# Kernel tuning notes

Hardware: AMD Instinct MI355X
Metric: run time of the kernel (lower is better)

## Reference

```python
import jax, jax.numpy as jnp
import numpy as np

E = 1_000_000      # edges in batch
N_BATCH = 50_000   # local nodes in batch
N_TOTAL = 100_000  # total entities
R = 1000           # num relations
D = 200            # rnn_in_dim == rnn_hid_dim


def setup_inputs() -> dict:
    key = jax.random.key(0)
    ks = jax.random.split(key, 9)
    s = 1.0 / np.sqrt(D)  # torch GRU init scale
    return {
        "edge_index": jax.random.randint(ks[0], (2, E), 0, N_BATCH),
        "edge_type": jax.random.randint(ks[1], (E,), 0, R),
        "node_id": jax.random.randint(ks[2], (N_BATCH,), 0, N_TOTAL),
        "static_entity_emb": jax.random.normal(ks[3], (N_TOTAL, D), jnp.float32),
        "dynamic_relation_emb": jax.random.normal(ks[4], (R, 1, D, 2), jnp.float32),
        "W_ih": jax.random.uniform(ks[5], (3 * D, D), jnp.float32, -s, s),
        "W_hh": jax.random.uniform(ks[6], (3 * D, D), jnp.float32, -s, s),
        "b_ih": jax.random.uniform(ks[7], (3 * D,), jnp.float32, -s, s),
        "b_hh": jax.random.uniform(ks[8], (3 * D,), jnp.float32, -s, s),
    }


def _scatter_mean_by_rel(emb, edge_type):
    # emb: [E, D] gathered entity embeddings; segment-mean over relation type -> [R, D]
    seg_sum = jax.ops.segment_sum(emb, edge_type, num_segments=R)
    cnt = jax.ops.segment_sum(jnp.ones((emb.shape[0], 1), emb.dtype), edge_type, num_segments=R)
    return jnp.where(cnt > 0, seg_sum / jnp.maximum(cnt, 1.0), 0.0)


def _gru_cell(x, h, W_ih, W_hh, b_ih, b_hh):
    # torch GRU gate order: r, z, n. x,h: [R, D]
    gi = x @ W_ih.T + b_ih
    gh = h @ W_hh.T + b_hh
    i_r, i_z, i_n = jnp.split(gi, 3, axis=-1)
    h_r, h_z, h_n = jnp.split(gh, 3, axis=-1)
    r = jax.nn.sigmoid(i_r + h_r)
    z = jax.nn.sigmoid(i_z + h_z)
    n = jnp.tanh(i_n + r * h_n)
    return (1.0 - z) * n + z * h


def reference(edge_index, edge_type, node_id, static_entity_emb,
              dynamic_relation_emb, W_ih, W_hh, b_ih, b_hh):
    src_nid = node_id[edge_index[0]]  # [E]
    dst_nid = node_id[edge_index[1]]  # [E]
    # gather + scatter-mean by relation (irregular access; the hot path)
    x_src = _scatter_mean_by_rel(static_entity_emb[src_nid], edge_type)  # [R, D]
    x_dst = _scatter_mean_by_rel(static_entity_emb[dst_nid], edge_type)  # [R, D]
    # single-layer hidden states per relation (side 0 = src, 1 = dst)
    h_src = dynamic_relation_emb[:, 0, :, 0]  # [R, D]
    h_dst = dynamic_relation_emb[:, 0, :, 1]  # [R, D]
    new_src = _gru_cell(x_src, h_src, W_ih, W_hh, b_ih, b_hh)
    new_dst = _gru_cell(x_dst, h_dst, W_ih, W_hh, b_ih, b_hh)
    # [R, num_layers=1, D, 2]
    return jnp.stack([new_src, new_dst], axis=-1)[:, None, :, :]
```

## Files before the change

kernel.cpp:

```cpp
#include <hip/hip_runtime.h>
#include <hip/hip_fp16.h>
#include <math.h>

#define DD     200
#define DD3    600
#define NBK    256
#define GB     256
#define SCH    8192
#define SCAP   11264
#define CHUNK  1024
#define KP     232
#define MP     2048
#define NP     640

typedef unsigned int   uint32;
typedef unsigned short uint16;
typedef __attribute__((ext_vector_type(8))) short bf16x8;
typedef __attribute__((ext_vector_type(4))) float f32x4;

static __device__ inline float bf2f(uint16 u) {
    union { uint32 i; float f; } x; x.i = ((uint32)u) << 16; return x.f;
}
static __device__ inline uint16 f2bf(float f) {
    union { float f; uint32 i; } x; x.f = f;
    return (uint16)((x.i + 0x7FFFu + ((x.i >> 16) & 1u)) >> 16);
}
static __device__ inline float asf(uint32 u) {
    union { uint32 i; float f; } x; x.i = u; return x.f;
}
static __device__ inline uint32 packbf(float a, float b) {
    return (uint32)f2bf(a) | ((uint32)f2bf(b) << 16);
}
static __device__ inline uint32 packh2(float a, float b) {
    __half2 h = __floats2half2_rn(a, b);
    union { __half2 h; uint32 u; } x; x.h = h; return x.u;
}
static __device__ inline __half2 ash2(uint32 u) {
    union { uint32 u; __half2 h; } x; x.u = u; return x.h;
}

__global__ void zero_kernel(int* __restrict__ cnt, int n) {
    int stride = gridDim.x * blockDim.x;
    for (int i = blockIdx.x * blockDim.x + threadIdx.x; i < n; i += stride) cnt[i] = 0;
}

__global__ void zerof_kernel(float* __restrict__ p, int n) {
    int stride = gridDim.x * blockDim.x;
    for (int i = blockIdx.x * blockDim.x + threadIdx.x; i < n; i += stride) p[i] = 0.f;
}

__launch_bounds__(512)
__global__ void blockhist_kernel(const int* __restrict__ etype, const int* __restrict__ eidx,
                                 int* __restrict__ boff, int E) {
    __shared__ int lc[NBK];
    const int tid = threadIdx.x;
    if (tid < NBK) lc[tid] = 0;
    __syncthreads();
    int per = (E + GB - 1) / GB;
    int beg = blockIdx.x * per;
    int end = min(E, beg + per);
    for (int e = beg + tid; e < end; e += 512) {
        int r  = etype[e];
        int ch = r >> 5;
        atomicAdd(&lc[(ch << 3) | (eidx[e] >> 13)], 1);
        atomicAdd(&lc[(ch << 3) | (eidx[E + e] >> 13)], 1);
    }
    __syncthreads();
    if (tid < NBK) boff[blockIdx.x * NBK + tid] = lc[tid];
}

__launch_bounds__(NBK)
__global__ void offscan_kernel(int* __restrict__ boff, int* __restrict__ offs256) {
    __shared__ int tot[NBK];
    __shared__ int s[NBK];
    const int t = threadIdx.x;
    int acc = 0;
    for (int b = 0; b < GB; ++b) {
        int v = boff[b * NBK + t];
        boff[b * NBK + t] = acc;
        acc += v;
    }
    tot[t] = acc;
    s[t] = acc;
    for (int off = 1; off < NBK; off <<= 1) {
        __syncthreads();
        int tmp = (t >= off) ? s[t - off] : 0;
        __syncthreads();
        s[t] += tmp;
    }
    __syncthreads();
    int base = s[t] - tot[t];
    offs256[t] = base;
    if (t == NBK - 1) offs256[NBK] = s[t];
    for (int b = 0; b < GB; ++b) boff[b * NBK + t] += base;
}

__launch_bounds__(512)
__global__ void blocksort_kernel(const int* __restrict__ etype, const int* __restrict__ eidx,
                                 const int* __restrict__ boff, uint32* __restrict__ binned,
                                 int E) {
    __shared__ uint32 raw[SCH];
    __shared__ uint32 srt[SCH];
    __shared__ int lhist[NBK];
    __shared__ int loff[NBK + 1];
    __shared__ int lcur[NBK];
    __shared__ int bbase[NBK];
    const int tid  = threadIdx.x;
    const int wv   = tid >> 6;
    const int lane = tid & 63;

    if (tid < NBK) bbase[tid] = boff[blockIdx.x * NBK + tid];
    int per = (E + GB - 1) / GB;
    int ebeg = blockIdx.x * per;
    int eend = min(E, ebeg + per);

    for (int cb = ebeg; cb < eend; cb += SCH / 2) {
        const int ne = min(SCH / 2, eend - cb);
        const int m  = 2 * ne;
        if (tid < NBK) lhist[tid] = 0;
        __syncthreads();
        for (int i = tid; i < ne; i += 512) {
            int e  = cb + i;
            int r  = etype[e];
            int sS = eidx[e];
            int sD = eidx[E + e];
            int ch = r >> 5;
            int rb = (r & 31) << 1;
            raw[2 * i]     = ((uint32)ch << 24) | ((uint32)rb << 16) | (uint32)sS;
            raw[2 * i + 1] = ((uint32)ch << 24) | ((uint32)(rb + 1) << 16) | (uint32)sD;
            atomicAdd(&lhist[(ch << 3) | (sS >> 13)], 1);
            atomicAdd(&lhist[(ch << 3) | (sD >> 13)], 1);
        }
        __syncthreads();
        if (tid == 0) {
            int acc = 0;
            for (int q = 0; q < NBK; ++q) { loff[q] = acc; acc += lhist[q]; }
            loff[NBK] = acc;
        }
        __syncthreads();
        if (tid < NBK) lcur[tid] = loff[tid];
        __syncthreads();
        for (int i = tid; i < m; i += 512) {
            uint32 pk = raw[i];
            int k = (int)((pk >> 24) << 3) | (int)((pk & 0xFFFFu) >> 13);
            int pos = atomicAdd(&lcur[k], 1);
            srt[pos] = pk;
        }
        __syncthreads();
        for (int b = wv; b < NBK; b += 8) {
            int lo = loff[b];
            int c  = loff[b + 1] - lo;
            if (c > 0) {
                int dst = bbase[b];
                for (int i = lane; i < c; i += 64) binned[dst + i] = srt[lo + i];
                if (lane == 0) bbase[b] = dst + c;
            }
        }
        __syncthreads();
    }
}

__launch_bounds__(512)
__global__ void sortbucket_kernel(const uint32* __restrict__ binned,
                                  const int* __restrict__ offs256,
                                  uint16* __restrict__ list, int* __restrict__ offs16k,
                                  int total) {
    __shared__ uint16 sorted[SCAP];
    __shared__ int hist[64];
    __shared__ int cur[64];
    __shared__ int scn[65];
    const int bk  = blockIdx.x;
    const int tid = threadIdx.x;
    const int beg = offs256[bk];
    const int end = offs256[bk + 1];
    const int len = end - beg;

    if (tid < 64) hist[tid] = 0;
    __syncthreads();
    for (int i = tid; i < len; i += 512)
        atomicAdd(&hist[(binned[beg + i] >> 16) & 63], 1);
    __syncthreads();
    if (tid == 0) {
        int acc = 0;
        #pragma unroll
        for (int q = 0; q < 64; ++q) { scn[q] = acc; cur[q] = acc; acc += hist[q]; }
        scn[64] = acc;
    }
    __syncthreads();
    if (tid < 64) offs16k[bk * 64 + tid] = beg + scn[tid];
    if (bk == 0 && tid == 64) offs16k[NBK * 64] = total;

    if (len <= SCAP) {
        for (int i = tid; i < len; i += 512) {
            uint32 e = binned[beg + i];
            int p = atomicAdd(&cur[(e >> 16) & 63], 1);
            sorted[p] = (uint16)(e & 0xFFFF);
        }
        __syncthreads();
        for (int i = tid; i < len; i += 512) list[beg + i] = sorted[i];
    } else {
        for (int i = tid; i < len; i += 512) {
            uint32 e = binned[beg + i];
            int p = atomicAdd(&cur[(e >> 16) & 63], 1);
            list[beg + p] = (uint16)(e & 0xFFFF);
        }
    }
}

__global__ void compact_kernel(const int* __restrict__ node_id, const float* __restrict__ emb,
                               uint32* __restrict__ cmp, int NB) {
    int idx = blockIdx.x * blockDim.x + threadIdx.x;
    if (idx >= NB * 50) return;
    int s = idx / 50, q = idx - s * 50;
    int nid = node_id[s];
    float4 v = *(const float4*)(emb + (size_t)nid * DD + 4 * q);
    *(uint2*)(cmp + (size_t)s * 100 + 2 * q) = make_uint2(packh2(v.x, v.y), packh2(v.z, v.w));
}

__launch_bounds__(256)
__global__ void partial7_kernel(const uint16* __restrict__ list,
                                const uint32* __restrict__ cmp,
                                const int* __restrict__ offs16k,
                                uint16* __restrict__ partial) {
    const int g    = blockIdx.x & 7;
    const int rest = blockIdx.x >> 3;
    const int rsl  = rest & 63;
    const int ch   = rest >> 6;
    const int b16  = ((ch * 8 + g) << 6) | rsl;
    const int tid  = threadIdx.x;
    const int w    = tid >> 6;
    const int lane = tid & 63;
    const int sub  = lane / 25;
    const int w25  = lane % 25;
    const int laneOff = w25 * 4;

    __shared__ uint16 sl[CHUNK];
    __shared__ float  red[8][DD];

    const int beg = offs16k[b16];
    const int end = offs16k[b16 + 1];

    __half2 h0 = __floats2half2_rn(0.f, 0.f);
    __half2 h1 = h0, h2 = h0, h3 = h0;

    for (int base = beg; base < end; base += CHUNK) {
        const int m = min(CHUNK, end - base);
        for (int i = tid; i < m; i += 256) sl[i] = list[base + i];
        __syncthreads();
        if (sub < 2) {
            int i = w * 2 + sub;
            for (; i + 24 < m; i += 32) {
                int s0 = sl[i];
                int s1 = sl[i + 8];
                int s2 = sl[i + 16];
                int s3 = sl[i + 24];
                uint4 v0 = *(const uint4*)(cmp + (size_t)s0 * 100 + laneOff);
                uint4 v1 = *(const uint4*)(cmp + (size_t)s1 * 100 + laneOff);
                uint4 v2 = *(const uint4*)(cmp + (size_t)s2 * 100 + laneOff);
                uint4 v3 = *(const uint4*)(cmp + (size_t)s3 * 100 + laneOff);
                h0 = __hadd2(h0, __hadd2(__hadd2(ash2(v0.x), ash2(v1.x)),
                                         __hadd2(ash2(v2.x), ash2(v3.x))));
                h1 = __hadd2(h1, __hadd2(__hadd2(ash2(v0.y), ash2(v1.y)),
                                         __hadd2(ash2(v2.y), ash2(v3.y))));
                h2 = __hadd2(h2, __hadd2(__hadd2(ash2(v0.z), ash2(v1.z)),
                                         __hadd2(ash2(v2.z), ash2(v3.z))));
                h3 = __hadd2(h3, __hadd2(__hadd2(ash2(v0.w), ash2(v1.w)),
                                         __hadd2(ash2(v2.w), ash2(v3.w))));
            }
            for (; i < m; i += 8) {
                int s0 = sl[i];
                uint4 v0 = *(const uint4*)(cmp + (size_t)s0 * 100 + laneOff);
                h0 = __hadd2(h0, ash2(v0.x));
                h1 = __hadd2(h1, ash2(v0.y));
                h2 = __hadd2(h2, ash2(v0.z));
                h3 = __hadd2(h3, ash2(v0.w));
            }
        }
        __syncthreads();
    }

    if (sub < 2) {
        int row = w * 2 + sub;
        int c = w25 * 8;
        red[row][c]     = __low2float(h0);  red[row][c + 1] = __high2float(h0);
        red[row][c + 2] = __low2float(h1);  red[row][c + 3] = __high2float(h1);
        red[row][c + 4] = __low2float(h2);  red[row][c + 5] = __high2float(h2);
        red[row][c + 6] = __low2float(h3);  red[row][c + 7] = __high2float(h3);
    }
    __syncthreads();

    if (tid < DD) {
        float s = 0.f;
        #pragma unroll
        for (int q = 0; q < 8; ++q) s += red[q][tid];
        partial[(size_t)b16 * DD + tid] = f2bf(s);
    }
}

__global__ void prep2_kernel(const uint16* __restrict__ partial,
                             const int* __restrict__ offs16k,
                             const float* __restrict__ dyn,
                             const float* __restrict__ W_ih, const float* __restrict__ W_hh,
                             uint32* __restrict__ Xb, uint32* __restrict__ Hb,
                             uint32* __restrict__ Wib, uint32* __restrict__ Whb, int RS2) {
    const int KU = KP / 2;
    int idx = blockIdx.x * blockDim.x + threadIdx.x;
    int XU = MP * KU, WU = NP * KU;
    const uint32* pp = (const uint32*)partial;
    if (idx < XU) {
        int row = idx / KU, kk = (idx - row * KU) * 2;
        uint32 o = 0;
        if (row < RS2 && kk < DD) {
            int ch = row >> 6, rsl = row & 63;
            float s0 = 0.f, s1 = 0.f;
            int n = 0;
            #pragma unroll
            for (int g = 0; g < 8; ++g) {
                int b16 = ((ch * 8 + g) << 6) | rsl;
                n += offs16k[b16 + 1] - offs16k[b16];
                uint32 v = pp[b16 * 100 + (kk >> 1)];
                s0 += asf(v << 16);
                s1 += asf(v & 0xFFFF0000u);
            }
            float rc = (n > 0) ? 1.f / (float)n : 0.f;
            o = packbf(s0 * rc, s1 * rc);
        }
        Xb[idx] = o;
    } else if (idx < 2 * XU) {
        int k2 = idx - XU;
        int row = k2 / KU, kk = (k2 - row * KU) * 2;
        uint32 o = 0;
        if (row < RS2 && kk < DD) {
            int r = row >> 1, side = row & 1;
            float h0 = dyn[((size_t)r * DD + kk) * 2 + side];
            float h1 = dyn[((size_t)r * DD + kk + 1) * 2 + side];
            o = packbf(h0, h1);
        }
        Hb[k2] = o;
    } else if (idx < 2 * XU + 2 * WU) {
        int k2 = idx - 2 * XU;
        const float* W = (k2 < WU) ? W_ih : W_hh;
        uint32* dst = (k2 < WU) ? Wib : Whb;
        if (k2 >= WU) k2 -= WU;
        int row = k2 / KU, kk = (k2 - row * KU) * 2;
        uint32 o = 0;
        if (row < DD3 && kk < DD) {
            o = packbf(W[(size_t)row * DD + kk], W[(size_t)row * DD + kk + 1]);
        }
        dst[k2] = o;
    }
}

__launch_bounds__(256)
__global__ void mfma_gates_kernel(const uint32* __restrict__ Xb, const uint32* __restrict__ Hb,
                                  const uint32* __restrict__ Wib, const uint32* __restrict__ Whb,
                                  float* __restrict__ G) {
    __shared__ short As[64 * KP];
    __shared__ short Bs[64 * KP];
    const int nt  = blockIdx.x;
    const int mt  = blockIdx.y;
    const int z   = blockIdx.z;
    const int tid = threadIdx.x;

    const uint32* Asrc = (z ? Hb : Xb) + (size_t)mt * 64 * (KP / 2);
    const uint32* Bsrc = (z ? Whb : Wib) + (size_t)nt * 64 * (KP / 2);
    {
        const uint4* a4 = (const uint4*)Asrc;
        const uint4* b4 = (const uint4*)Bsrc;
        uint4* la = (uint4*)As;
        uint4* lb = (uint4*)Bs;
        const int n16 = 64 * KP * 2 / 16;
        for (int i = tid; i < n16; i += 256) { la[i] = a4[i]; lb[i] = b4[i]; }
    }
    __syncthreads();

    const int w    = tid >> 6;
    const int lane = tid & 63;
    const int qm   = (w & 1) * 32;
    const int qn   = (w >> 1) * 32;
    const int lr   = lane & 15;
    const int lk   = (lane >> 4) * 8;

    f32x4 acc00 = {0.f, 0.f, 0.f, 0.f}, acc01 = acc00, acc10 = acc00, acc11 = acc00;
    #pragma unroll
    for (int ks = 0; ks < 7; ++ks) {
        int kof = ks * 32 + lk;
        bf16x8 a0 = *(const bf16x8*)&As[(qm + lr) * KP + kof];
        bf16x8 a1 = *(const bf16x8*)&As[(qm + 16 + lr) * KP + kof];
        bf16x8 b0 = *(const bf16x8*)&Bs[(qn + lr) * KP + kof];
        bf16x8 b1 = *(const bf16x8*)&Bs[(qn + 16 + lr) * KP + kof];
        acc00 = __builtin_amdgcn_mfma_f32_16x16x32_bf16(a0, b0, acc00, 0, 0, 0);
        acc01 = __builtin_amdgcn_mfma_f32_16x16x32_bf16(a0, b1, acc01, 0, 0, 0);
        acc10 = __builtin_amdgcn_mfma_f32_16x16x32_bf16(a1, b0, acc10, 0, 0, 0);
        acc11 = __builtin_amdgcn_mfma_f32_16x16x32_bf16(a1, b1, acc11, 0, 0, 0);
    }

    float* Gz = G + (size_t)z * MP * NP;
    const int mb = mt * 64 + qm + (lane >> 4) * 4;
    const int nb = nt * 64 + qn + lr;
    #pragma unroll
    for (int r = 0; r < 4; ++r) {
        Gz[(size_t)(mb + r) * NP + nb]           = acc00[r];
        Gz[(size_t)(mb + r) * NP + nb + 16]      = acc01[r];
        Gz[(size_t)(mb + 16 + r) * NP + nb]      = acc10[r];
        Gz[(size_t)(mb + 16 + r) * NP + nb + 16] = acc11[r];
    }
}

__global__ void gruf2_kernel(const float* __restrict__ G, const float* __restrict__ dyn,
                             const float* __restrict__ b_ih, const float* __restrict__ b_hh,
                             float* __restrict__ out, int RS2) {
    int idx = blockIdx.x * blockDim.x + threadIdx.x;
    int total = RS2 * DD;
    if (idx >= total) return;
    int rs = idx / DD, t = idx - rs * DD;
    int r = rs >> 1, side = rs & 1;
    const float* Gi = G;
    const float* Gh = G + (size_t)MP * NP;
    size_t base = (size_t)rs * NP;
    float ga   = Gi[base + t]          + b_ih[t]          + Gh[base + t]          + b_hh[t];
    float gz   = Gi[base + DD + t]     + b_ih[DD + t]     + Gh[base + DD + t]     + b_hh[DD + t];
    float gi_n = Gi[base + 2 * DD + t] + b_ih[2 * DD + t];
    float gh_n = Gh[base + 2 * DD + t] + b_hh[2 * DD + t];
    float rg = 1.f / (1.f + __expf(-ga));
    float zz = 1.f / (1.f + __expf(-gz));
    float nn = tanhf(gi_n + rg * gh_n);
    float h  = dyn[((size_t)r * DD + t) * 2 + side];
    out[((size_t)r * DD + t) * 2 + side] = (1.f - zz) * nn + zz * h;
}

__global__ void hist_kernel(const int* __restrict__ etype, int* __restrict__ cnt,
                            int E, int R) {
    __shared__ int lc[1024];
    for (int i = threadIdx.x; i < R; i += blockDim.x) lc[i] = 0;
    __syncthreads();
    int stride = gridDim.x * blockDim.x;
    for (int i = blockIdx.x * blockDim.x + threadIdx.x; i < E; i += stride)
        atomicAdd(&lc[etype[i]], 1);
    __syncthreads();
    for (int i = threadIdx.x; i < R; i += blockDim.x)
        if (lc[i]) atomicAdd(&cnt[i], lc[i]);
}

__global__ void atomic_acc_kernel(const int* __restrict__ eidx, const int* __restrict__ etype,
                                  const int* __restrict__ node_id, const float* __restrict__ emb,
                                  float* __restrict__ acc, int E) {
    int gtid = blockIdx.x * blockDim.x + threadIdx.x;
    int wave = gtid >> 6, lane = gtid & 63;
    int nwaves = (gridDim.x * blockDim.x) >> 6;
    for (int e = wave; e < E; e += nwaves) {
        int r = etype[e];
        float* dst = acc + (size_t)r * DD * 2;
        for (int side = 0; side < 2; ++side) {
            int nid = node_id[eidx[(size_t)side * E + e]];
            const float* row = emb + (size_t)nid * DD;
            for (int d = lane; d < DD; d += 64)
                atomicAdd(&dst[d * 2 + side], row[d]);
        }
    }
}

__launch_bounds__(256)
__global__ void gru_inplace_kernel(const float* __restrict__ dyn, const float* __restrict__ W_ih,
                                   const float* __restrict__ W_hh, const float* __restrict__ b_ih,
                                   const float* __restrict__ b_hh, const int* __restrict__ cnt,
                                   float* __restrict__ out) {
    const int r = blockIdx.x, side = blockIdx.y, tid = threadIdx.x;
    __shared__ float xs[DD], hs[DD], gi[DD3], gh[DD3];
    if (tid < DD) {
        float s = out[((size_t)r * DD + tid) * 2 + side];
        int n = cnt[r];
        xs[tid] = (n > 0) ? s / (float)n : 0.f;
        hs[tid] = dyn[((size_t)r * DD + tid) * 2 + side];
    }
    __syncthreads();
    for (int jj = tid; jj < DD3; jj += 256) {
        float a = b_ih[jj], c = b_hh[jj];
        const float* rI = W_ih + (size_t)jj * DD;
        const float* rH = W_hh + (size_t)jj * DD;
        for (int k = 0; k < DD; ++k) { a = fmaf(xs[k], rI[k], a); c = fmaf(hs[k], rH[k], c); }
        gi[jj] = a; gh[jj] = c;
    }
    __syncthreads();
    if (tid < DD) {
        float rr = 1.f / (1.f + __expf(-(gi[tid] + gh[tid])));
        float zz = 1.f / (1.f + __expf(-(gi[DD + tid] + gh[DD + tid])));
        float nn = tanhf(gi[2 * DD + tid] + rr * gh[2 * DD + tid]);
        out[((size_t)r * DD + tid) * 2 + side] = (1.f - zz) * nn + zz * hs[tid];
    }
}

extern "C" void kernel_launch(void* const* d_in, const int* in_sizes, int n_in,
                              void* d_out, int out_size, void* d_ws, size_t ws_size,
                              hipStream_t stream) {
    const int*   eidx    = (const int*)d_in[0];
    const int*   etype   = (const int*)d_in[1];
    const int*   node_id = (const int*)d_in[2];
    const float* emb     = (const float*)d_in[3];
    const float* dyn     = (const float*)d_in[4];
    const float* W_ih    = (const float*)d_in[5];
    const float* W_hh    = (const float*)d_in[6];
    const float* b_ih    = (const float*)d_in[7];
    const float* b_hh    = (const float*)d_in[8];
    float*       out     = (float*)d_out;

    const int E   = in_sizes[1];
    const int NB  = in_sizes[2];
    const int D   = in_sizes[7] / 3;
    const int R   = in_sizes[4] / (2 * D);
    const int RS2 = R * 2;

    char* p = (char*)d_ws;
    auto take = [&](size_t bytes) { char* q = p; p += (bytes + 255) & ~(size_t)255; return q; };
    int*    boff    = (int*)   take((size_t)GB * NBK * 4);
    int*    offs256 = (int*)   take((size_t)(NBK + 1) * 4);
    int*    offs16k = (int*)   take((size_t)(NBK * 64 + 1) * 4);
    uint32* cmp     = (uint32*)take((size_t)NB * 100 * 4);
    uint16* list    = (uint16*)take((size_t)2 * E * 2);
    uint16* partial = (uint16*)take((size_t)NBK * 64 * DD * 2);
    size_t need_full = (size_t)(p - (char*)d_ws);

    uint32* binned = cmp;
    float*  G      = (float*)cmp;
    const int KU = KP / 2;
    uint32* Xb  = (uint32*)list;
    uint32* Hb  = Xb + (size_t)MP * KU;
    uint32* Wib = Hb + (size_t)MP * KU;
    uint32* Whb = Wib + (size_t)NP * KU;
    size_t ovl_list = (size_t)(2 * MP + 2 * NP) * KU * 4;
    size_t ovl_cmp1 = (size_t)2 * E * 4;
    size_t ovl_cmp2 = (size_t)2 * MP * NP * 4;
    const bool overlay_ok = (ovl_list <= (size_t)2 * E * 2) &&
                            (ovl_cmp1 <= (size_t)NB * 100 * 4) &&
                            (ovl_cmp2 <= (size_t)NB * 100 * 4);

    const bool fits = (ws_size >= need_full) && (NB <= 50000) && (R == 1000) &&
                      (D == 200) && overlay_ok && (E <= 1000000);
    if (fits) {
        blockhist_kernel<<<GB, 512, 0, stream>>>(etype, eidx, boff, E);
        offscan_kernel<<<1, NBK, 0, stream>>>(boff, offs256);
        blocksort_kernel<<<GB, 512, 0, stream>>>(etype, eidx, boff, binned, E);
        sortbucket_kernel<<<NBK, 512, 0, stream>>>(binned, offs256, list, offs16k, 2 * E);
        compact_kernel<<<(NB * 50 + 255) / 256, 256, 0, stream>>>(node_id, emb, cmp, NB);
        partial7_kernel<<<NBK * 64, 256, 0, stream>>>(list, cmp, offs16k, partial);
        int ptot = 2 * MP * KU + 2 * NP * KU;
        prep2_kernel<<<(ptot + 255) / 256, 256, 0, stream>>>(partial, offs16k, dyn, W_ih, W_hh,
                                                             Xb, Hb, Wib, Whb, RS2);
        dim3 mg(NP / 64, MP / 64, 2);
        mfma_gates_kernel<<<mg, 256, 0, stream>>>(Xb, Hb, Wib, Whb, G);
        gruf2_kernel<<<(RS2 * DD + 255) / 256, 256, 0, stream>>>(G, dyn, b_ih, b_hh, out, RS2);
    } else {
        int* cnt = (int*)d_ws;
        zero_kernel<<<32, 256, 0, stream>>>(cnt, R);
        hist_kernel<<<512, 256, 0, stream>>>(etype, cnt, E, R);
        zerof_kernel<<<(R * D * 2 + 255) / 256, 256, 0, stream>>>(out, R * D * 2);
        atomic_acc_kernel<<<2048, 256, 0, stream>>>(eidx, etype, node_id, emb, out, E);
        dim3 grid(R, 2);
        gru_inplace_kernel<<<grid, 256, 0, stream>>>(dyn, W_ih, W_hh, b_ih, b_hh, cnt, out);
    }
}
```

Baseline: 145.8 us.

## Parallelize offset scans across blocks and replace serial shared-memory scans

The single-block offset scan, which walked 256 block rows serially and ran over the array twice, is split into two kernels. One uses 256 blocks, each scanning one bucket column across source blocks, and a tiny kernel then scans the bucket totals. The blocksort kernel adds the global bucket base when it loads its offsets. The single-thread serial prefix sums inside blocksort and sortbucket are replaced with parallel Hillis-Steele scans in shared memory. This adds one kernel launch and more barriers in exchange for removing serial latency chains.

Result: faster. 122.8 us (-15.8%).

```diff
diff --git a/kernel.cpp b/kernel.cpp
--- a/kernel.cpp
+++ b/kernel.cpp
@@ -69,47 +69,57 @@
     if (tid < NBK) boff[blockIdx.x * NBK + tid] = lc[tid];
 }
 
+__launch_bounds__(GB)
+__global__ void offscanA_kernel(int* __restrict__ boff, int* __restrict__ tot) {
+    __shared__ int s[GB];
+    const int g   = blockIdx.x;
+    const int tid = threadIdx.x;
+    int v = boff[(size_t)tid * NBK + g];
+    s[tid] = v;
+    for (int off = 1; off < GB; off <<= 1) {
+        __syncthreads();
+        int t2 = (tid >= off) ? s[tid - off] : 0;
+        __syncthreads();
+        s[tid] += t2;
+    }
+    __syncthreads();
+    boff[(size_t)tid * NBK + g] = s[tid] - v;
+    if (tid == GB - 1) tot[g] = s[tid];
+}
+
 __launch_bounds__(NBK)
-__global__ void offscan_kernel(int* __restrict__ boff, int* __restrict__ offs256) {
-    __shared__ int tot[NBK];
+__global__ void offscanB_kernel(const int* __restrict__ tot, int* __restrict__ offs256) {
     __shared__ int s[NBK];
     const int t = threadIdx.x;
-    int acc = 0;
-    for (int b = 0; b < GB; ++b) {
-        int v = boff[b * NBK + t];
-        boff[b * NBK + t] = acc;
-        acc += v;
-    }
-    tot[t] = acc;
-    s[t] = acc;
+    int v = tot[t];
+    s[t] = v;
     for (int off = 1; off < NBK; off <<= 1) {
         __syncthreads();
-        int tmp = (t >= off) ? s[t - off] : 0;
-        __syncthreads();
-        s[t] += tmp;
-    }
-    __syncthreads();
-    int base = s[t] - tot[t];
-    offs256[t] = base;
+        int t2 = (t >= off) ? s[t - off] : 0;
+        __syncthreads();
+        s[t] += t2;
+    }
+    __syncthreads();
+    offs256[t] = s[t] - v;
     if (t == NBK - 1) offs256[NBK] = s[t];
-    for (int b = 0; b < GB; ++b) boff[b * NBK + t] += base;
 }
 
 __launch_bounds__(512)
 __global__ void blocksort_kernel(const int* __restrict__ etype, const int* __restrict__ eidx,
-                                 const int* __restrict__ boff, uint32* __restrict__ binned,
-                                 int E) {
+                                 const int* __restrict__ boff, const int* __restrict__ offs256,
+                                 uint32* __restrict__ binned, int E) {
     __shared__ uint32 raw[SCH];
     __shared__ uint32 srt[SCH];
     __shared__ int lhist[NBK];
     __shared__ int loff[NBK + 1];
     __shared__ int lcur[NBK];
     __shared__ int bbase[NBK];
+    __shared__ int sc[NBK];
     const int tid  = threadIdx.x;
     const int wv   = tid >> 6;
     const int lane = tid & 63;
 
-    if (tid < NBK) bbase[tid] = boff[blockIdx.x * NBK + tid];
+    if (tid < NBK) bbase[tid] = boff[blockIdx.x * NBK + tid] + offs256[tid];
     int per = (E + GB - 1) / GB;
     int ebeg = blockIdx.x * per;
     int eend = min(E, ebeg + per);
@@ -132,13 +142,19 @@
             atomicAdd(&lhist[(ch << 3) | (sD >> 13)], 1);
         }
         __syncthreads();
-        if (tid == 0) {
-            int acc = 0;
-            for (int q = 0; q < NBK; ++q) { loff[q] = acc; acc += lhist[q]; }
-            loff[NBK] = acc;
-        }
-        __syncthreads();
-        if (tid < NBK) lcur[tid] = loff[tid];
+        if (tid < NBK) sc[tid] = lhist[tid];
+        for (int off = 1; off < NBK; off <<= 1) {
+            __syncthreads();
+            int t2 = (tid < NBK && tid >= off) ? sc[tid - off] : 0;
+            __syncthreads();
+            if (tid < NBK) sc[tid] += t2;
+        }
+        __syncthreads();
+        if (tid < NBK) {
+            loff[tid] = sc[tid] - lhist[tid];
+            lcur[tid] = loff[tid];
+            if (tid == NBK - 1) loff[NBK] = sc[tid];
+        }
         __syncthreads();
         for (int i = tid; i < m; i += 512) {
             uint32 pk = raw[i];
@@ -169,6 +185,7 @@
     __shared__ int hist[64];
     __shared__ int cur[64];
     __shared__ int scn[65];
+    __shared__ int sc[64];
     const int bk  = blockIdx.x;
     const int tid = threadIdx.x;
     const int beg = offs256[bk];
@@ -180,11 +197,18 @@
     for (int i = tid; i < len; i += 512)
         atomicAdd(&hist[(binned[beg + i] >> 16) & 63], 1);
     __syncthreads();
-    if (tid == 0) {
-        int acc = 0;
-        #pragma unroll
-        for (int q = 0; q < 64; ++q) { scn[q] = acc; cur[q] = acc; acc += hist[q]; }
-        scn[64] = acc;
+    if (tid < 64) sc[tid] = hist[tid];
+    for (int off = 1; off < 64; off <<= 1) {
+        __syncthreads();
+        int t2 = (tid < 64 && tid >= off) ? sc[tid - off] : 0;
+        __syncthreads();
+        if (tid < 64) sc[tid] += t2;
+    }
+    __syncthreads();
+    if (tid < 64) {
+        scn[tid] = sc[tid] - hist[tid];
+        cur[tid] = scn[tid];
+        if (tid == 63) scn[64] = sc[63];
     }
     __syncthreads();
     if (tid < 64) offs16k[bk * 64 + tid] = beg + scn[tid];
@@ -513,6 +537,7 @@
     char* p = (char*)d_ws;
     auto take = [&](size_t bytes) { char* q = p; p += (bytes + 255) & ~(size_t)255; return q; };
     int*    boff    = (int*)   take((size_t)GB * NBK * 4);
+    int*    tot     = (int*)   take((size_t)NBK * 4);
     int*    offs256 = (int*)   take((size_t)(NBK + 1) * 4);
     int*    offs16k = (int*)   take((size_t)(NBK * 64 + 1) * 4);
     uint32* cmp     = (uint32*)take((size_t)NB * 100 * 4);
@@ -538,8 +563,9 @@
                       (D == 200) && overlay_ok && (E <= 1000000);
     if (fits) {
         blockhist_kernel<<<GB, 512, 0, stream>>>(etype, eidx, boff, E);
-        offscan_kernel<<<1, NBK, 0, stream>>>(boff, offs256);
-        blocksort_kernel<<<GB, 512, 0, stream>>>(etype, eidx, boff, binned, E);
+        offscanA_kernel<<<NBK, GB, 0, stream>>>(boff, tot);
+        offscanB_kernel<<<1, NBK, 0, stream>>>(tot, offs256);
+        blocksort_kernel<<<GB, 512, 0, stream>>>(etype, eidx, boff, offs256, binned, E);
         sortbucket_kernel<<<NBK, 512, 0, stream>>>(binned, offs256, list, offs16k, 2 * E);
         compact_kernel<<<(NB * 50 + 255) / 256, 256, 0, stream>>>(node_id, emb, cmp, NB);
         partial7_kernel<<<NBK * 64, 256, 0, stream>>>(list, cmp, offs16k, partial);
```
